# Kernel tuning notes

Hardware: AMD Instinct MI355X
Metric: run time of the kernel (lower is better)

The kernel has to match this reference:

```python
import jax, jax.numpy as jnp
import numpy as np
import math

B, T, D, H, V = 32, 512, 256, 4, 5000
NL = 6          # transformer layers
DUR_CAP = 8     # cap per-token duration so output length is static under jit
T_OUT = 2048    # fixed regulated length (avg duration ~1-2 with small init)


def _layernorm(x, g, b, eps=1e-5):
    m = jnp.mean(x, axis=-1, keepdims=True)
    v = jnp.var(x, axis=-1, keepdims=True)
    return (x - m) * jax.lax.rsqrt(v + eps) * g + b


def _conv1d(x, w, b):
    # x [B,C,T], w [O,I,K] -> [B,O,T], 'same' padding as in torch
    pad = (w.shape[-1] - 1) // 2
    y = jax.lax.conv_general_dilated(x, w, (1,), [(pad, pad)],
                                     dimension_numbers=('NCH', 'OIH', 'NCH'))
    return y + b[None, :, None]


def _pos_encoding(t, d):
    pos = jnp.arange(t, dtype=jnp.float32)[:, None]
    div = jnp.exp(jnp.arange(0, d, 2, dtype=jnp.float32) * (-math.log(10000.0) / d))
    ang = pos * div  # [t, d/2]
    return jnp.stack([jnp.sin(ang), jnp.cos(ang)], axis=-1).reshape(t, d)


def setup_inputs():
    key = jax.random.key(0)
    ks = iter(jax.random.split(key, 64))
    def nrm(shape, s=0.02):
        return jax.random.normal(next(ks), shape, dtype=jnp.float32) * s
    return {
        'text': jax.random.randint(next(ks), (B, T), 0, V, dtype=jnp.int32),
        'emotion': jax.random.normal(next(ks), (B, 1), dtype=jnp.float32),
        'emb': nrm((V, D), 1.0),
        'Wqkv': nrm((NL, D, 3 * D)), 'bqkv': jnp.zeros((NL, 3 * D)),
        'Wo': nrm((NL, D, D)), 'bo': jnp.zeros((NL, D)),
        'W1': nrm((NL, D, 4 * D)), 'b1': jnp.zeros((NL, 4 * D)),
        'W2': nrm((NL, 4 * D, D)), 'b2': jnp.zeros((NL, D)),
        'ln1g': jnp.ones((NL, D)), 'ln1b': jnp.zeros((NL, D)),
        'ln2g': jnp.ones((NL, D)), 'ln2b': jnp.zeros((NL, D)),
        'We1': nrm((1, 64), 0.1), 'be1': jnp.zeros((64,)),
        'We2': nrm((64, D), 0.1), 'be2': jnp.zeros((D,)),
        'dp_w1': nrm((D, D, 3)), 'dp_b1': jnp.zeros((D,)),
        'dp_g1': jnp.ones((D,)), 'dp_bt1': jnp.zeros((D,)),
        'dp_m1': jnp.zeros((D,)), 'dp_v1': jnp.ones((D,)),
        'dp_w2': nrm((D, D, 3)), 'dp_b2': jnp.zeros((D,)),
        'dp_g2': jnp.ones((D,)), 'dp_bt2': jnp.zeros((D,)),
        'dp_m2': jnp.zeros((D,)), 'dp_v2': jnp.ones((D,)),
        'dp_wo': nrm((1, D, 1)), 'dp_bo': jnp.zeros((1,)),
        'dec_w1': nrm((256, D, 5)), 'dec_b1': jnp.zeros((256,)),
        'dec_w2': nrm((128, 256, 5)), 'dec_b2': jnp.zeros((128,)),
        'dec_w3': nrm((1, 128, 5)), 'dec_b3': jnp.zeros((1,)),
    }


def reference(text, emotion, emb, Wqkv, bqkv, Wo, bo, W1, b1, W2, b2,
              ln1g, ln1b, ln2g, ln2b, We1, be1, We2, be2,
              dp_w1, dp_b1, dp_g1, dp_bt1, dp_m1, dp_v1,
              dp_w2, dp_b2, dp_g2, dp_bt2, dp_m2, dp_v2, dp_wo, dp_bo,
              dec_w1, dec_b1, dec_w2, dec_b2, dec_w3, dec_b3):
    dh = D // H
    scale = 1.0 / math.sqrt(dh)
    x = emb[text] + _pos_encoding(T, D)[None]  # [B,T,D]
    # post-norm TransformerEncoder (torch default), relu FFN, eval mode
    for i in range(NL):
        qkv = x @ Wqkv[i] + bqkv[i]
        q, k, v = jnp.split(qkv, 3, axis=-1)
        q = q.reshape(B, T, H, dh); k = k.reshape(B, T, H, dh); v = v.reshape(B, T, H, dh)
        att = jax.nn.softmax(jnp.einsum('bthd,bshd->bhts', q, k) * scale, axis=-1)
        o = jnp.einsum('bhts,bshd->bthd', att, v).reshape(B, T, D) @ Wo[i] + bo[i]
        x = _layernorm(x + o, ln1g[i], ln1b[i])
        ff = jax.nn.relu(x @ W1[i] + b1[i]) @ W2[i] + b2[i]
        x = _layernorm(x + ff, ln2g[i], ln2b[i])
    # EmotionFusion (assumed additive MLP projection, output_dim = 256)
    e = jax.nn.relu(emotion @ We1 + be1) @ We2 + be2  # [B,256]
    fused = x + e[:, None, :]                          # [B,T,D]
    # DurationPredictor (eval: BN with running stats, dropout off)
    def bn(y, g, bt, m, vv):
        return g[None, :, None] * (y - m[None, :, None]) * jax.lax.rsqrt(vv + 1e-5)[None, :, None] + bt[None, :, None]
    h = fused.transpose(0, 2, 1)  # [B,D,T]
    h = bn(jax.nn.relu(_conv1d(h, dp_w1, dp_b1)), dp_g1, dp_bt1, dp_m1, dp_v1)
    h = bn(jax.nn.relu(_conv1d(h, dp_w2, dp_b2)), dp_g2, dp_bt2, dp_m2, dp_v2)
    log_dur = _conv1d(h, dp_wo, dp_bo)[:, 0, :]  # [B,T]
    dur = jnp.clip(jnp.round(jnp.exp(log_dur)), 1, DUR_CAP).astype(jnp.int32)
    dur = jax.lax.stop_gradient(dur)
    # LengthRegulator: repeat token i dur[i] times, zero-pad to T_OUT
    def regulate(xb, db):
        total = jnp.sum(db)
        pad = jnp.maximum(T_OUT - total, 0)
        xe = jnp.concatenate([xb, jnp.zeros((1, D), xb.dtype)], axis=0)
        de = jnp.concatenate([db, pad[None]], axis=0)
        return jnp.repeat(xe, de, axis=0, total_repeat_length=T_OUT)
    reg = jax.vmap(regulate)(fused, dur)  # [B,T_OUT,D]
    # decoder conv stack
    y = reg.transpose(0, 2, 1)
    y = jax.nn.relu(_conv1d(y, dec_w1, dec_b1))
    y = jax.nn.relu(_conv1d(y, dec_w2, dec_b2))
    wav = _conv1d(y, dec_w3, dec_b3)[:, 0, :]  # [B,T_OUT]
    return wav
```

## Files before the change

kernel.cpp:

```cpp
#include <hip/hip_runtime.h>
#include <math.h>

#define NB 32
#define NT 512
#define ND 256
#define NH 4
#define NLAYER 6
#define TOUT 2048

typedef __attribute__((ext_vector_type(8))) short bf16x8;
typedef __attribute__((ext_vector_type(4))) float f32x4;
typedef __attribute__((ext_vector_type(16))) float f32x16;

static __device__ __forceinline__ unsigned short f2b(float f) {
    union { float f; unsigned int u; } x; x.f = f;
    unsigned int u = x.u;
    return (unsigned short)((u + 0x7FFFu + ((u >> 16) & 1u)) >> 16);
}
static __device__ __forceinline__ float b2f(unsigned short s) {
    union { unsigned int u; float f; } x; x.u = ((unsigned int)s) << 16;
    return x.f;
}

#define OFF_X    0ull
#define OFF_FFH  4194304ull
#define OFF_WBT  12582912ull
#define OFF_CWT  14942208ull
#define OFF_QKV  20971520ull
#define OFF_ATTN 33554432ull
#define OFF_PROJ 37748736ull
#define OFF_E    41943040ull
#define OFF_INT  41951232ull

__global__ __launch_bounds__(256) void embed_kernel(const int* __restrict__ text,
                                                    const float* __restrict__ emb,
                                                    float* __restrict__ x)
{
    const int row = blockIdx.x;
    const int d = threadIdx.x;
    const int t = row & (NT - 1);
    const int id = text[row];
    const int j2 = (d >> 1) * 2;
    const float c = -9.210340371976184f / 256.0f;
    float freq = expf((float)j2 * c);
    float ang = (float)t * freq;
    float pe = (d & 1) ? cosf(ang) : sinf(ang);
    x[(size_t)row * ND + d] = emb[(size_t)id * ND + d] + pe;
}

__global__ __launch_bounds__(256) void wq_kernel(const float* __restrict__ W,
                                                 unsigned short* __restrict__ out,
                                                 int K, int N, int inLS, int outLS)
{
    __shared__ float tile[32][33];
    const float* Wl = W + (size_t)blockIdx.z * inLS;
    unsigned short* ol = out + (size_t)blockIdx.z * outLS;
    const int n0 = blockIdx.x * 32, k0 = blockIdx.y * 32;
    const int tx = threadIdx.x & 31, ty = threadIdx.x >> 5;
#pragma unroll
    for (int j = 0; j < 4; ++j)
        tile[ty + j * 8][tx] = Wl[(size_t)(k0 + ty + j * 8) * N + n0 + tx];
    __syncthreads();
#pragma unroll
    for (int j = 0; j < 4; ++j)
        ol[(size_t)(n0 + ty + j * 8) * K + k0 + tx] = f2b(tile[tx][ty + j * 8]);
}

template<int NTILE, bool RELU, bool ABF16, bool CBF16>
__global__ __launch_bounds__(256) void gemmbf_kernel(const void* __restrict__ A_,
                                                     const unsigned short* __restrict__ Bt,
                                                     const float* __restrict__ bias,
                                                     void* __restrict__ C_,
                                                     int M, int N, int K)
{
    constexpr int MT = (NTILE == 128) ? 2 : 1;
    __shared__ __align__(16) unsigned short Asb[128 * 32];
    __shared__ __align__(16) unsigned short Bsb[NTILE * 32];
    const int tid = threadIdx.x;
    const int lane = tid & 63, wave = tid >> 6;
    const int ln = lane & 31, hi = lane >> 5;
    const int row0 = blockIdx.y * 128, col0 = blockIdx.x * NTILE;
    const int mOff = (NTILE == 128) ? (wave >> 1) * 64 : wave * 32;
    const int nOff = (NTILE == 128) ? (wave & 1) * 64 : 0;
    const float* Af = (const float*)A_;
    const unsigned short* Ab = (const unsigned short*)A_;
    float* Cf = (float*)C_;
    unsigned short* Cb = (unsigned short*)C_;
// ... 1 lines not shown

    for (int k0 = 0; k0 < K; k0 += 32) {
#pragma unroll
        for (int it = 0; it < 2; ++it) {
            int u = it * 256 + tid;
            int m = u >> 2, blk = u & 3;
            unsigned short s8[8];
            if (ABF16) {
                *(uint4*)s8 = *(const uint4*)&Ab[(size_t)(row0 + m) * K + k0 + blk * 8];
            } else {
                float4 v0 = *(const float4*)&Af[(size_t)(row0 + m) * K + k0 + blk * 8];
                float4 v1 = *(const float4*)&Af[(size_t)(row0 + m) * K + k0 + blk * 8 + 4];
                s8[0] = f2b(v0.x); s8[1] = f2b(v0.y); s8[2] = f2b(v0.z); s8[3] = f2b(v0.w);
                s8[4] = f2b(v1.x); s8[5] = f2b(v1.y); s8[6] = f2b(v1.z); s8[7] = f2b(v1.w);
            }
            *(uint4*)&Asb[m * 32 + ((blk ^ (m & 3)) << 3)] = *(uint4*)s8;
        }
#pragma unroll
        for (int it = 0; it < NTILE / 64; ++it) {
            int u = it * 256 + tid;
            int n = u >> 2, blk = u & 3;
            *(uint4*)&Bsb[n * 32 + ((blk ^ (n & 3)) << 3)] =
                *(const uint4*)&Bt[(size_t)(col0 + n) * K + k0 + blk * 8];
        }
        __syncthreads();
#pragma unroll
        for (int kh = 0; kh < 2; ++kh) {
            const int kb = kh * 2 + hi;
            bf16x8 af[MT], bfr[2];
#pragma unroll
            for (int mt = 0; mt < MT; ++mt) {
                int r = mOff + mt * 32 + ln;
                af[mt] = *(const bf16x8*)&Asb[r * 32 + ((kb ^ (r & 3)) << 3)];
            }
#pragma unroll
            for (int nt = 0; nt < 2; ++nt) {
                int r = nOff + nt * 32 + ln;
                bfr[nt] = *(const bf16x8*)&Bsb[r * 32 + ((kb ^ (r & 3)) << 3)];
            }
#pragma unroll
            for (int mt = 0; mt < MT; ++mt)
#pragma unroll
                for (int nt = 0; nt < 2; ++nt)
                    acc[mt][nt] = __builtin_amdgcn_mfma_f32_32x32x16_bf16(
                        af[mt], bfr[nt], acc[mt][nt], 0, 0, 0);
        }
        __syncthreads();
    }
#pragma unroll
    for (int mt = 0; mt < MT; ++mt)
#pragma unroll
        for (int nt = 0; nt < 2; ++nt) {
            int col = col0 + nOff + nt * 32 + ln;
            float bi = bias[col];
#pragma unroll
            for (int g = 0; g < 4; ++g)
#pragma unroll
                for (int r4 = 0; r4 < 4; ++r4) {
                    int row = row0 + mOff + mt * 32 + hi * 4 + g * 8 + r4;
                    float v = acc[mt][nt][g * 4 + r4] + bi;
                    if (RELU) v = fmaxf(v, 0.f);
                    if (CBF16) Cb[(size_t)row * N + col] = f2b(v);
                    else       Cf[(size_t)row * N + col] = v;
                }
        }
}

__global__ __launch_bounds__(256) void vtrans_kernel(const unsigned short* __restrict__ qkv,
                                                     unsigned short* __restrict__ vt)
{
    __shared__ unsigned short tile[64][65];
    const int t0 = blockIdx.x * 64, h = blockIdx.y, b = blockIdx.z;
    const int tid = threadIdx.x;
#pragma unroll
    for (int it = 0; it < 2; ++it) {
        int u = it * 256 + tid;
        int t = u >> 3, d8 = (u & 7) * 8;
        bf16x8 v = *(const bf16x8*)&qkv[((size_t)(b * NT) + t0 + t) * 768 + 512 + h * 64 + d8];
#pragma unroll
        for (int j = 0; j < 8; ++j) tile[t][d8 + j] = (unsigned short)v[j];
    }
    __syncthreads();
#pragma unroll
    for (int it = 0; it < 2; ++it) {
        int u = it * 256 + tid;
        int d = u >> 3, t8 = (u & 7) * 8;
        unsigned short s8[8];
#pragma unroll
        for (int j = 0; j < 8; ++j) s8[j] = tile[t8 + j][d];
        *(uint4*)&vt[((size_t)(b * NH + h) * 64 + d) * NT + t0 + t8] = *(uint4*)s8;
    }
}

__global__ __launch_bounds__(256, 2) void attn3_kernel(const unsigned short* __restrict__ qkv,
                                                       const unsigned short* __restrict__ vt,
                                                       unsigned short* __restrict__ out)
{
    __shared__ __align__(16) unsigned short sP[4][32 * 64];
    const int tid = threadIdx.x;
    const int lane = tid & 63, wave = tid >> 6;
    const int ln = lane & 31, hi = lane >> 5;
    const int h = blockIdx.y, b = blockIdx.z;
    const int q0 = blockIdx.x * 128 + wave * 32;
    const size_t base = (size_t)b * NT * 768;
    const int qoff = h * 64;
    const unsigned short* vbh = vt + (size_t)(b * NH + h) * 64 * NT;
// ... 100 lines not shown
#pragma unroll
    for (int o = 1; o < 64; o <<= 1) s += __shfl_xor(s, o);
    float m = s * (1.0f / 256.0f);
    float4 dv = make_float4(v.x - m, v.y - m, v.z - m, v.w - m);
    float s2 = dv.x * dv.x + dv.y * dv.y + dv.z * dv.z + dv.w * dv.w;
#pragma unroll
    for (int o = 1; o < 64; o <<= 1) s2 += __shfl_xor(s2, o);
    float r = 1.0f / sqrtf(s2 * (1.0f / 256.0f) + 1e-5f);
    float4 gv = *(const float4*)&g[c4];
    float4 bv = *(const float4*)&bta[c4];
    float4 o4 = make_float4(dv.x * r * gv.x + bv.x, dv.y * r * gv.y + bv.y,
                            dv.z * r * gv.z + bv.z, dv.w * r * gv.w + bv.w);
    *(float4*)&x[row * ND + c4] = o4;
}

__global__ __launch_bounds__(256) void emotion_kernel(const float* __restrict__ emo,
                                                      const float* __restrict__ We1,
                                                      const float* __restrict__ be1,
                                                      const float* __restrict__ We2,
                                                      const float* __restrict__ be2,
                                                      float* __restrict__ e)
{
    const int b = blockIdx.x, d = threadIdx.x;
    const float em = emo[b];
    float acc = be2[d];
    for (int j = 0; j < 64; ++j) {
        float h = fmaxf(em * We1[j] + be1[j], 0.0f);
        acc = fmaf(h, We2[j * ND + d], acc);
    }
    e[b * ND + d] = acc;
}

__global__ __launch_bounds__(256) void addfuse_kernel(float* __restrict__ x,
                                                      const float* __restrict__ e)
{
    const int row = blockIdx.x;
    const int d = threadIdx.x;
    x[(size_t)row * ND + d] += e[(row >> 9) * ND + d];
}

__global__ __launch_bounds__(256) void wtrans_kernel(const float* __restrict__ w,
                                                     float* __restrict__ wt,
                                                     int CIN, int COUT, int KS)
{
    int gid = blockIdx.x * 256 + threadIdx.x;
    int total = CIN * COUT * KS;
    if (gid >= total) return;
    int o = gid % COUT;
    int r = gid / COUT;
    int c = r % CIN;
    int k = r / CIN;
    wt[gid] = w[(o * CIN + c) * KS + k];
}

__global__ __launch_bounds__(256) void wtransb_kernel(const float* __restrict__ w,
                                                      unsigned short* __restrict__ wtb,
                                                      int CIN, int COUT, int KS)
{
    int gid = blockIdx.x * 256 + threadIdx.x;
    int total = CIN * COUT * KS;
    if (gid >= total) return;
    int c = gid % CIN;
    int r = gid / CIN;
    int o = r % COUT;
    int k = r / COUT;
    wtb[gid] = f2b(w[(o * CIN + c) * KS + k]);
}

template<int CIN, int KS, bool RELU, bool BN, bool GATHER>
__global__ __launch_bounds__(256, 4) void convg_kernel(const float* __restrict__ in,
                                                       const float* __restrict__ wt,
                                                       const float* __restrict__ bias,
                                                       const float* __restrict__ bng,
                                                       const float* __restrict__ bnb,
                                                       const float* __restrict__ bnm,
                                                       const float* __restrict__ bnv,
                                                       const int* __restrict__ tok,
                                                       float* __restrict__ out,
                                                       int T, int in_T, int COUT)
{
    constexpr int TM = 128;
    constexpr int PAD = (KS - 1) / 2;
    constexpr int TEXT = TM + KS - 1;
    constexpr int PITCH = (TEXT + 3) & ~3;
    __shared__ __align__(16) float As[16 * PITCH];
    __shared__ __align__(16) float Bs[16 * KS * 68];
    const int tid = threadIdx.x;
    const int lane = tid & 63, wave = tid >> 6;
    const int b = blockIdx.z;
    const int t0 = blockIdx.x * TM;
    const int o0 = blockIdx.y * 64;
    const int wt0 = wave * 32;
    const int r0 = (lane >> 3) << 2;
    const int c0 = (lane & 7) << 2;
    float acc[4][8] = {};

    for (int cc = 0; cc < CIN; cc += 16) {
        for (int i = tid; i < TEXT * 4; i += 256) {
            int t = i >> 2, q = i & 3;
            int tg = t0 - PAD + t;
            float4 v = make_float4(0.f, 0.f, 0.f, 0.f);
            if (tg >= 0 && tg < T) {
                long row;
                if (GATHER) {
                    int tk = tok[b * T + tg];
                    row = (tk >= 0) ? ((long)b * in_T + tk) : -1;
                } else {
                    row = (long)b * T + tg;
                }
                if (row >= 0) v = *(const float4*)&in[row * CIN + cc + (q << 2)];
            }
            As[((q << 2) + 0) * PITCH + t] = v.x;
            As[((q << 2) + 1) * PITCH + t] = v.y;
            As[((q << 2) + 2) * PITCH + t] = v.z;
            As[((q << 2) + 3) * PITCH + t] = v.w;
        }
        for (int i = tid; i < KS * 256; i += 256) {
            int row = i >> 4, o4 = (i & 15) << 2;
            int k = row >> 4, ci = row & 15;
            *(float4*)&Bs[row * 68 + o4] =
                *(const float4*)&wt[(size_t)(k * CIN + cc + ci) * COUT + o0 + o4];
        }
        __syncthreads();
#pragma unroll 2
        for (int ci = 0; ci < 16; ++ci) {
            float a[8];
            float4 A0 = *(const float4*)&As[ci * PITCH + wt0 + r0];
            float4 A1 = *(const float4*)&As[ci * PITCH + wt0 + r0 + 4];
            a[0] = A0.x; a[1] = A0.y; a[2] = A0.z; a[3] = A0.w;
            a[4] = A1.x; a[5] = A1.y; a[6] = A1.z; a[7] = A1.w;
#pragma unroll
            for (int k = 0; k < KS; ++k) {
                float4 b0 = *(const float4*)&Bs[(k * 16 + ci) * 68 + c0];
                float4 b1 = *(const float4*)&Bs[(k * 16 + ci) * 68 + 32 + c0];
                float bb[8] = {b0.x, b0.y, b0.z, b0.w, b1.x, b1.y, b1.z, b1.w};
#pragma unroll
                for (int i = 0; i < 4; ++i)
#pragma unroll
                    for (int j = 0; j < 8; ++j)
                        acc[i][j] = fmaf(a[i + k], bb[j], acc[i][j]);
            }
        }
        __syncthreads();
    }

    float4 bi0 = *(const float4*)(bias + o0 + c0);
    float4 bi1 = *(const float4*)(bias + o0 + 32 + c0);
    float bb[8] = {bi0.x, bi0.y, bi0.z, bi0.w, bi1.x, bi1.y, bi1.z, bi1.w};
    float sc[8], sh[8];
    if (BN) {
        float4 g0 = *(const float4*)(bng + o0 + c0);
        float4 g1 = *(const float4*)(bng + o0 + 32 + c0);
        float4 t0v = *(const float4*)(bnb + o0 + c0);
        float4 t1v = *(const float4*)(bnb + o0 + 32 + c0);
        float4 m0 = *(const float4*)(bnm + o0 + c0);
        float4 m1 = *(const float4*)(bnm + o0 + 32 + c0);
        float4 v0 = *(const float4*)(bnv + o0 + c0);
        float4 v1 = *(const float4*)(bnv + o0 + 32 + c0);
        float gg[8] = {g0.x, g0.y, g0.z, g0.w, g1.x, g1.y, g1.z, g1.w};
        float tb[8] = {t0v.x, t0v.y, t0v.z, t0v.w, t1v.x, t1v.y, t1v.z, t1v.w};
        float mm[8] = {m0.x, m0.y, m0.z, m0.w, m1.x, m1.y, m1.z, m1.w};
        float vv[8] = {v0.x, v0.y, v0.z, v0.w, v1.x, v1.y, v1.z, v1.w};
#pragma unroll
        for (int j = 0; j < 8; ++j) {
            sc[j] = gg[j] / sqrtf(vv[j] + 1e-5f);
            sh[j] = tb[j] - mm[j] * sc[j];
        }
    }
#pragma unroll
    for (int i = 0; i < 4; ++i) {
        int r = t0 + wt0 + r0 + i;
#pragma unroll
        for (int jh = 0; jh < 2; ++jh) {
            float o4[4];
#pragma unroll
            for (int j = 0; j < 4; ++j) {
                float yv = acc[i][jh * 4 + j] + bb[jh * 4 + j];
                if (RELU) yv = fmaxf(yv, 0.0f);
                if (BN) yv = yv * sc[jh * 4 + j] + sh[jh * 4 + j];
                o4[j] = yv;
            }
            *(float4*)&out[((size_t)b * T + r) * COUT + o0 + jh * 32 + c0] =
                make_float4(o4[0], o4[1], o4[2], o4[3]);
        }
    }
}

__global__ __launch_bounds__(256) void reg_kernel(const float* __restrict__ x,
                                                  const int* __restrict__ tok,
                                                  unsigned short* __restrict__ reg)
{
    const int wave = threadIdx.x >> 6, lane = threadIdx.x & 63;
    const int row = blockIdx.x * 4 + wave;
    const int tk = tok[row];
    const int b = row >> 11;
    const int c4 = lane * 4;
    unsigned short s4[4] = {0, 0, 0, 0};
    if (tk >= 0) {
        float4 v = *(const float4*)&x[((size_t)(b * NT) + tk) * ND + c4];
        s4[0] = f2b(v.x); s4[1] = f2b(v.y); s4[2] = f2b(v.z); s4[3] = f2b(v.w);
    }
    *(uint2*)&reg[(size_t)row * ND + c4] = *(uint2*)s4;
}

template<int CIN, int KS, bool RELU>
__global__ __launch_bounds__(256) void convmf2_kernel(const unsigned short* __restrict__ in,
                                                      const unsigned short* __restrict__ wtb,
                                                      const float* __restrict__ bias,
                                                      unsigned short* __restrict__ out,
                                                      int T, int COUT)
{
    constexpr int PAD = (KS - 1) / 2;
    constexpr int TEXT = 128 + KS - 1;
    __shared__ __align__(16) unsigned short Asb[TEXT * 32];
    __shared__ __align__(16) unsigned short Bsb[KS * 64 * 32];
    const int tid = threadIdx.x;
    const int lane = tid & 63, wave = tid >> 6;
    const int ln = lane & 31, hi = lane >> 5;
    const int b = blockIdx.z;
    const int t0 = blockIdx.x * 128;
    const int o0 = blockIdx.y * 64;
    const int mOff = wave * 32;
    f32x16 acc[2] = {};

    for (int cc = 0; cc < CIN; cc += 32) {
        for (int u = tid; u < TEXT * 4; u += 256) {
            int t = u >> 2, blk = u & 3;
            int tg = t0 - PAD + t;
            uint4 v = make_uint4(0, 0, 0, 0);
            if (tg >= 0 && tg < T)
                v = *(const uint4*)&in[((size_t)(b * T) + tg) * CIN + cc + blk * 8];
            *(uint4*)&Asb[t * 32 + ((blk ^ (t & 3)) << 3)] = v;
        }
        for (int u = tid; u < KS * 256; u += 256) {
            int row = u >> 2, blk = u & 3;
            int k = row >> 6, o = row & 63;
            *(uint4*)&Bsb[row * 32 + ((blk ^ (row & 3)) << 3)] =
                *(const uint4*)&wtb[((size_t)k * COUT + o0 + o) * CIN + cc + blk * 8];
        }
        __syncthreads();
#pragma unroll
        for (int kh = 0; kh < 2; ++kh) {
            const int kb = kh * 2 + hi;
            bf16x8 af[KS];
#pragma unroll
            for (int tap = 0; tap < KS; ++tap) {
                int r = mOff + ln + tap;
                af[tap] = *(const bf16x8*)&Asb[r * 32 + ((kb ^ (r & 3)) << 3)];
            }
#pragma unroll
            for (int nt = 0; nt < 2; ++nt) {
                int rb = nt * 32 + ln;
#pragma unroll
                for (int tap = 0; tap < KS; ++tap) {
                    bf16x8 bfr = *(const bf16x8*)&Bsb[(tap * 64 + rb) * 32 + ((kb ^ (rb & 3)) << 3)];
                    acc[nt] = __builtin_amdgcn_mfma_f32_32x32x16_bf16(af[tap], bfr, acc[nt], 0, 0, 0);
                }
            }
        }
        __syncthreads();
    }
#pragma unroll
    for (int nt = 0; nt < 2; ++nt) {
        int col = o0 + nt * 32 + ln;
        float bi = bias[col];
#pragma unroll
        for (int g = 0; g < 4; ++g)
#pragma unroll
            for (int r4 = 0; r4 < 4; ++r4) {
                int row = t0 + mOff + hi * 4 + g * 8 + r4;
                float v = acc[nt][g * 4 + r4] + bi;
                if (RELU) v = fmaxf(v, 0.f);
                out[((size_t)(b * T) + row) * COUT + col] = f2b(v);
            }
    }
}

__global__ __launch_bounds__(256) void dur_kernel(const float* __restrict__ h2,
                                                  const float* __restrict__ wo,
                                                  const float* __restrict__ bo,
                                                  int* __restrict__ dur)
{
    const int wave = threadIdx.x >> 6, lane = threadIdx.x & 63;
    const int row = blockIdx.x * 4 + wave;
    const int c4 = lane * 4;
    float4 h = *(const float4*)&h2[(size_t)row * ND + c4];
    float4 w4 = *(const float4*)&wo[c4];
    float s = h.x * w4.x + h.y * w4.y + h.z * w4.z + h.w * w4.w;
#pragma unroll
    for (int o = 1; o < 64; o <<= 1) s += __shfl_xor(s, o);
    if (lane == 0) {
        float d = rintf(expf(s + bo[0]));
        d = fminf(fmaxf(d, 1.0f), 8.0f);
        dur[row] = (int)d;
    }
}

__global__ __launch_bounds__(64) void scan_kernel(const int* __restrict__ dur,
                                                  int* __restrict__ starts,
                                                  int* __restrict__ totals)
{
    const int b = threadIdx.x;
    if (b >= NB) return;
    int acc = 0;
    for (int t = 0; t < NT; ++t) {
        starts[b * NT + t] = acc;
        acc += dur[b * NT + t];
    }
    totals[b] = acc;
}

__global__ __launch_bounds__(256) void tok_kernel(const int* __restrict__ starts,
                                                  const int* __restrict__ totals,
                                                  int* __restrict__ tok)
{
    const int gid = blockIdx.x * 256 + threadIdx.x;
    const int b = gid >> 11, p = gid & (TOUT - 1);
    const int total = totals[b];
    int res = -1;
    if (p < total) {
        const int* st = starts + b * NT;
        int lo = 0, hi = NT - 1;
        while (lo < hi) {
            int mid = (lo + hi + 1) >> 1;
            if (st[mid] <= p) lo = mid; else hi = mid - 1;
        }
        res = lo;
    }
    tok[gid] = res;
}

__global__ __launch_bounds__(256) void conv3_kernel(const unsigned short* __restrict__ in,
                                                    const float* __restrict__ w,
                                                    const float* __restrict__ bias,
                                                    float* __restrict__ out)
{
    const int wave = threadIdx.x >> 6, lane = threadIdx.x & 63;
    const int gid = blockIdx.x * 4 + wave;
    const int b = gid >> 11, t = gid & (TOUT - 1);
    const int c = lane * 2;
    float w0[5], w1[5];
#pragma unroll
    for (int k = 0; k < 5; ++k) { w0[k] = w[c * 5 + k]; w1[k] = w[(c + 1) * 5 + k]; }
    float acc = 0.f;
// ... 35 lines not shown
    const float* be2     = (const float*)d_in[18];
    const float* dp_w1   = (const float*)d_in[19];
    const float* dp_b1   = (const float*)d_in[20];
    const float* dp_g1   = (const float*)d_in[21];
    const float* dp_bt1  = (const float*)d_in[22];
    const float* dp_m1   = (const float*)d_in[23];
    const float* dp_v1   = (const float*)d_in[24];
    const float* dp_w2   = (const float*)d_in[25];
    const float* dp_b2   = (const float*)d_in[26];
    const float* dp_g2   = (const float*)d_in[27];
    const float* dp_bt2  = (const float*)d_in[28];
    const float* dp_m2   = (const float*)d_in[29];
    const float* dp_v2   = (const float*)d_in[30];
    const float* dp_wo   = (const float*)d_in[31];
    const float* dp_bo   = (const float*)d_in[32];
    const float* dec_w1  = (const float*)d_in[33];
    const float* dec_b1  = (const float*)d_in[34];
    const float* dec_w2  = (const float*)d_in[35];
    const float* dec_b2  = (const float*)d_in[36];
    const float* dec_w3  = (const float*)d_in[37];
    const float* dec_b3  = (const float*)d_in[38];

    float* ws   = (float*)d_ws;
    float* x    = ws + OFF_X;
    unsigned short* ffhB = (unsigned short*)(ws + OFF_FFH);
    unsigned short* Wbt  = (unsigned short*)(ws + OFF_WBT);
    float* wtdp1 = ws + OFF_CWT;
    float* wtdp2 = wtdp1 + 196608;
    unsigned short* wtb1 = (unsigned short*)(wtdp2 + 196608);
    unsigned short* wtb2 = wtb1 + 327680;
    unsigned short* qkvB = (unsigned short*)(ws + OFF_QKV);
    unsigned short* vtb  = qkvB + 12582912;
    unsigned short* regB = qkvB;
    float* attb = ws + OFF_ATTN;
    float* prjb = ws + OFF_PROJ;
    float* ebuf = ws + OFF_E;
    unsigned short* attbB = (unsigned short*)attb;
    unsigned short* d1b  = ffhB;
    unsigned short* d2b  = (unsigned short*)attb;
    int*   ip     = (int*)(ws + OFF_INT);
    int*   durb   = ip;
    int*   startb = ip + 16384;
    int*   totb   = ip + 32768;
    int*   tokb   = ip + 32832;

    const int M = NB * NT;

    embed_kernel<<<M, 256, 0, stream>>>(text, emb, x);

    wq_kernel<<<dim3(24, 8, 6), 256, 0, stream>>>(Wqkv, Wbt + 0,      256, 768,  196608, 786432);
    wq_kernel<<<dim3(8,  8, 6), 256, 0, stream>>>(Wo,   Wbt + 196608, 256, 256,  65536,  786432);
    wq_kernel<<<dim3(32, 8, 6), 256, 0, stream>>>(W1,   Wbt + 262144, 256, 1024, 262144, 786432);
    wq_kernel<<<dim3(8, 32, 6), 256, 0, stream>>>(W2,   Wbt + 524288, 1024, 256, 262144, 786432);

    for (int l = 0; l < NLAYER; ++l) {
        const unsigned short* WQ  = Wbt + (size_t)l * 786432;
        const unsigned short* WO  = WQ + 196608;
        const unsigned short* WF1 = WQ + 262144;
        const unsigned short* WF2 = WQ + 524288;
        gemmbf_kernel<128, false, false, true><<<dim3(6, 128), 256, 0, stream>>>(
            x, WQ, bqkv + l * 768, qkvB, M, 768, 256);
        vtrans_kernel<<<dim3(NT / 64, NH, NB), 256, 0, stream>>>(qkvB, vtb);
        attn3_kernel<<<dim3(NT / 128, NH, NB), 256, 0, stream>>>(qkvB, vtb, attbB);
        gemmbf_kernel<64, false, true, false><<<dim3(4, 128), 256, 0, stream>>>(
            attbB, WO, bo + l * 256, prjb, M, 256, 256);
        add_ln_kernel<<<M / 4, 256, 0, stream>>>(x, prjb, ln1g + l * ND, ln1b + l * ND);
        gemmbf_kernel<128, true, false, true><<<dim3(8, 128), 256, 0, stream>>>(
            x, WF1, b1 + l * 1024, ffhB, M, 1024, 256);
        gemmbf_kernel<64, false, true, false><<<dim3(4, 128), 256, 0, stream>>>(
            ffhB, WF2, b2 + l * 256, prjb, M, 256, 1024);
        add_ln_kernel<<<M / 4, 256, 0, stream>>>(x, prjb, ln2g + l * ND, ln2b + l * ND);
    }

    emotion_kernel<<<NB, 256, 0, stream>>>(emotion, We1, be1, We2, be2, ebuf);
    addfuse_kernel<<<M, 256, 0, stream>>>(x, ebuf);

    wtrans_kernel<<<(256 * 256 * 3 + 255) / 256, 256, 0, stream>>>(dp_w1, wtdp1, 256, 256, 3);
    wtrans_kernel<<<(256 * 256 * 3 + 255) / 256, 256, 0, stream>>>(dp_w2, wtdp2, 256, 256, 3);
    wtransb_kernel<<<(256 * 256 * 5 + 255) / 256, 256, 0, stream>>>(dec_w1, wtb1, 256, 256, 5);
    wtransb_kernel<<<(128 * 256 * 5 + 255) / 256, 256, 0, stream>>>(dec_w2, wtb2, 256, 128, 5);

    convg_kernel<256, 3, true, true, false><<<dim3(NT / 128, 4, NB), 256, 0, stream>>>(
        x, wtdp1, dp_b1, dp_g1, dp_bt1, dp_m1, dp_v1, nullptr, attb, NT, NT, 256);
    convg_kernel<256, 3, true, true, false><<<dim3(NT / 128, 4, NB), 256, 0, stream>>>(
        attb, wtdp2, dp_b2, dp_g2, dp_bt2, dp_m2, dp_v2, nullptr, prjb, NT, NT, 256);
    dur_kernel<<<M / 4, 256, 0, stream>>>(prjb, dp_wo, dp_bo, durb);
    scan_kernel<<<1, 64, 0, stream>>>(durb, startb, totb);
    tok_kernel<<<NB * TOUT / 256, 256, 0, stream>>>(startb, totb, tokb);

    reg_kernel<<<NB * TOUT / 4, 256, 0, stream>>>(x, tokb, regB);
    convmf2_kernel<256, 5, true><<<dim3(TOUT / 128, 4, NB), 256, 0, stream>>>(
        regB, wtb1, dec_b1, d1b, TOUT, 256);
    convmf2_kernel<256, 5, true><<<dim3(TOUT / 128, 2, NB), 256, 0, stream>>>(
        d1b, wtb2, dec_b2, d2b, TOUT, 128);
    conv3_kernel<<<NB * TOUT / 4, 256, 0, stream>>>(d2b, dec_w3, dec_b3, (float*)d_out);
}
```

Measured before the change: 1.619 ms.

## Fuse V transpose into QKV GEMM, move duration convs to MFMA, merge prep kernels

The QKV GEMM epilogue now writes V directly in transposed layout, which removes the separate vtrans kernel. The fp32 duration-predictor convolutions are replaced by a unified bf16 MFMA conv kernel that is also used for the decoder convs. Weight-prep launches are merged into single kernels, emotion is fused into the add, and scan plus token lookup become one per-batch kernel. The LDS swizzle in the GEMM also changes. Together these cut launch count and memory traffic, at the cost of bf16 precision in the duration path, which could flip rounded durations.

```diff
diff --git a/kernel.cpp b/kernel.cpp
--- a/kernel.cpp
+++ b/kernel.cpp
@@ -21,6 +21,8 @@
     union { unsigned int u; float f; } x; x.u = ((unsigned int)s) << 16;
     return x.f;
 }
+
+#define SW(r) (((r) >> 1) & 3)
 
 #define OFF_X    0ull
 #define OFF_FFH  4194304ull
@@ -29,7 +31,6 @@
 #define OFF_QKV  20971520ull
 #define OFF_ATTN 33554432ull
 #define OFF_PROJ 37748736ull
-#define OFF_E    41943040ull
 #define OFF_INT  41951232ull
 
 __global__ __launch_bounds__(256) void embed_kernel(const int* __restrict__ text,
@@ -48,14 +49,21 @@
     x[(size_t)row * ND + d] = emb[(size_t)id * ND + d] + pe;
 }
 
-__global__ __launch_bounds__(256) void wq_kernel(const float* __restrict__ W,
-                                                 unsigned short* __restrict__ out,
-                                                 int K, int N, int inLS, int outLS)
+__global__ __launch_bounds__(256) void wqall_kernel(const float* __restrict__ Wqkv,
+                                                    const float* __restrict__ Wo,
+                                                    const float* __restrict__ W1,
+                                                    const float* __restrict__ W2,
+                                                    unsigned short* __restrict__ Wbt)
 {
     __shared__ float tile[32][33];
-    const float* Wl = W + (size_t)blockIdx.z * inLS;
-    unsigned short* ol = out + (size_t)blockIdx.z * outLS;
-    const int n0 = blockIdx.x * 32, k0 = blockIdx.y * 32;
+    const int tt = blockIdx.x, layer = blockIdx.y;
+    const float* src; int K, N, n0, k0, inLS; size_t outSeg;
+    if (tt < 192)      { src = Wqkv; K = 256;  N = 768;  n0 = (tt % 24) * 32; k0 = (tt / 24) * 32; inLS = 196608; outSeg = 0; }
+    else if (tt < 256) { int t2 = tt - 192; src = Wo; K = 256; N = 256;  n0 = (t2 & 7) * 32;  k0 = (t2 >> 3) * 32; inLS = 65536;  outSeg = 196608; }
+    else if (tt < 512) { int t3 = tt - 256; src = W1; K = 256; N = 1024; n0 = (t3 & 31) * 32; k0 = (t3 >> 5) * 32; inLS = 262144; outSeg = 262144; }
+    else               { int t4 = tt - 512; src = W2; K = 1024; N = 256; n0 = (t4 & 7) * 32;  k0 = (t4 >> 3) * 32; inLS = 262144; outSeg = 524288; }
+    const float* Wl = src + (size_t)layer * inLS;
+    unsigned short* ol = Wbt + (size_t)layer * 786432 + outSeg;
     const int tx = threadIdx.x & 31, ty = threadIdx.x >> 5;
 #pragma unroll
     for (int j = 0; j < 4; ++j)
@@ -66,11 +74,32 @@
         ol[(size_t)(n0 + ty + j * 8) * K + k0 + tx] = f2b(tile[tx][ty + j * 8]);
 }
 
-template<int NTILE, bool RELU, bool ABF16, bool CBF16>
+__global__ __launch_bounds__(256) void wtransball_kernel(const float* __restrict__ dp_w1,
+                                                         const float* __restrict__ dp_w2,
+                                                         const float* __restrict__ dec_w1,
+                                                         const float* __restrict__ dec_w2,
+                                                         unsigned short* __restrict__ cw)
+{
+    int gid = blockIdx.x * 256 + threadIdx.x;
+    if (gid >= 884736) return;
+    const float* src; int CIN = 256, COUT, KS, idx;
+    if (gid < 196608)      { src = dp_w1;  COUT = 256; KS = 3; idx = gid; }
+    else if (gid < 393216) { src = dp_w2;  COUT = 256; KS = 3; idx = gid - 196608; }
+    else if (gid < 720896) { src = dec_w1; COUT = 256; KS = 5; idx = gid - 393216; }
+    else                   { src = dec_w2; COUT = 128; KS = 5; idx = gid - 720896; }
+    int c = idx % CIN;
+    int r = idx / CIN;
+    int o = r % COUT;
+    int k = r / COUT;
+    cw[gid] = f2b(src[(o * CIN + c) * KS + k]);
+}
+
+template<int NTILE, bool RELU, bool ABF16, bool CBF16, bool VOUT>
 __global__ __launch_bounds__(256) void gemmbf_kernel(const void* __restrict__ A_,
                                                      const unsigned short* __restrict__ Bt,
                                                      const float* __restrict__ bias,
                                                      void* __restrict__ C_,
+                                                     unsigned short* __restrict__ vt,
                                                      int M, int N, int K)
 {
     constexpr int MT = (NTILE == 128) ? 2 : 1;
@@ -102,13 +131,13 @@
                 s8[0] = f2b(v0.x); s8[1] = f2b(v0.y); s8[2] = f2b(v0.z); s8[3] = f2b(v0.w);
                 s8[4] = f2b(v1.x); s8[5] = f2b(v1.y); s8[6] = f2b(v1.z); s8[7] = f2b(v1.w);
             }
-            *(uint4*)&Asb[m * 32 + ((blk ^ (m & 3)) << 3)] = *(uint4*)s8;
+            *(uint4*)&Asb[m * 32 + ((blk ^ SW(m)) << 3)] = *(uint4*)s8;
         }
 #pragma unroll
         for (int it = 0; it < NTILE / 64; ++it) {
             int u = it * 256 + tid;
             int n = u >> 2, blk = u & 3;
-            *(uint4*)&Bsb[n * 32 + ((blk ^ (n & 3)) << 3)] =
+            *(uint4*)&Bsb[n * 32 + ((blk ^ SW(n)) << 3)] =
                 *(const uint4*)&Bt[(size_t)(col0 + n) * K + k0 + blk * 8];
         }
         __syncthreads();
@@ -119,12 +148,12 @@
 #pragma unroll
             for (int mt = 0; mt < MT; ++mt) {
                 int r = mOff + mt * 32 + ln;
-                af[mt] = *(const bf16x8*)&Asb[r * 32 + ((kb ^ (r & 3)) << 3)];
+                af[mt] = *(const bf16x8*)&Asb[r * 32 + ((kb ^ SW(r)) << 3)];
             }
 #pragma unroll
             for (int nt = 0; nt < 2; ++nt) {
                 int r = nOff + nt * 32 + ln;
-                bfr[nt] = *(const bf16x8*)&Bsb[r * 32 + ((kb ^ (r & 3)) << 3)];
+                bfr[nt] = *(const bf16x8*)&Bsb[r * 32 + ((kb ^ SW(r)) << 3)];
             }
 #pragma unroll
             for (int mt = 0; mt < MT; ++mt)
@@ -142,42 +171,24 @@
             int col = col0 + nOff + nt * 32 + ln;
             float bi = bias[col];
 #pragma unroll
-            for (int g = 0; g < 4; ++g)
+            for (int g = 0; g < 4; ++g) {
+                unsigned short s4[4];
 #pragma unroll
                 for (int r4 = 0; r4 < 4; ++r4) {
                     int row = row0 + mOff + mt * 32 + hi * 4 + g * 8 + r4;
                     float v = acc[mt][nt][g * 4 + r4] + bi;
                     if (RELU) v = fmaxf(v, 0.f);
-                    if (CBF16) Cb[(size_t)row * N + col] = f2b(v);
+                    if (CBF16) { s4[r4] = f2b(v); Cb[(size_t)row * N + col] = s4[r4]; }
                     else       Cf[(size_t)row * N + col] = v;
                 }
-        }
-}
-
-__global__ __launch_bounds__(256) void vtrans_kernel(const unsigned short* __restrict__ qkv,
-                                                     unsigned short* __restrict__ vt)
-{
-    __shared__ unsigned short tile[64][65];
-    const int t0 = blockIdx.x * 64, h = blockIdx.y, b = blockIdx.z;
-    const int tid = threadIdx.x;
-#pragma unroll
-    for (int it = 0; it < 2; ++it) {
-        int u = it * 256 + tid;
-        int t = u >> 3, d8 = (u & 7) * 8;
-        bf16x8 v = *(const bf16x8*)&qkv[((size_t)(b * NT) + t0 + t) * 768 + 512 + h * 64 + d8];
-#pragma unroll
-        for (int j = 0; j < 8; ++j) tile[t][d8 + j] = (unsigned short)v[j];
-    }
-    __syncthreads();
-#pragma unroll
-    for (int it = 0; it < 2; ++it) {
-        int u = it * 256 + tid;
-        int d = u >> 3, t8 = (u & 7) * 8;
-        unsigned short s8[8];
-#pragma unroll
-        for (int j = 0; j < 8; ++j) s8[j] = tile[t8 + j][d];
-        *(uint4*)&vt[((size_t)(b * NH + h) * 64 + d) * NT + t0 + t8] = *(uint4*)s8;
-    }
+                if (VOUT && col >= 512) {
+                    int rowg = row0 + mOff + mt * 32 + hi * 4 + g * 8;
+                    int b = rowg >> 9, t = rowg & (NT - 1);
+                    int hh = (col - 512) >> 6, dd = (col - 512) & 63;
+                    *(uint2*)&vt[((size_t)(b * NH + hh) * 64 + dd) * NT + t] = *(uint2*)s4;
+                }
+            }
+        }
 }
 
 __global__ __launch_bounds__(256, 2) void attn3_kernel(const unsigned short* __restrict__ qkv,
@@ -308,201 +319,34 @@
     *(float4*)&x[row * ND + c4] = o4;
 }
 
-__global__ __launch_bounds__(256) void emotion_kernel(const float* __restrict__ emo,
-                                                      const float* __restrict__ We1,
-                                                      const float* __restrict__ be1,
-                                                      const float* __restrict__ We2,
-                                                      const float* __restrict__ be2,
-                                                      float* __restrict__ e)
-{
-    const int b = blockIdx.x, d = threadIdx.x;
-    const float em = emo[b];
+__global__ __launch_bounds__(256) void fuse_kernel(const float* __restrict__ emo,
+                                                   const float* __restrict__ We1,
+                                                   const float* __restrict__ be1,
+                                                   const float* __restrict__ We2,
+                                                   const float* __restrict__ be2,
+                                                   float* __restrict__ x)
+{
+    const int row = blockIdx.x;
+    const int d = threadIdx.x;
+    const float em = emo[row >> 9];
     float acc = be2[d];
     for (int j = 0; j < 64; ++j) {
         float h = fmaxf(em * We1[j] + be1[j], 0.0f);
         acc = fmaf(h, We2[j * ND + d], acc);
     }
-    e[b * ND + d] = acc;
-}
-
-__global__ __launch_bounds__(256) void addfuse_kernel(float* __restrict__ x,
-                                                      const float* __restrict__ e)
-{
-    const int row = blockIdx.x;
-    const int d = threadIdx.x;
-    x[(size_t)row * ND + d] += e[(row >> 9) * ND + d];
-}
-
-__global__ __launch_bounds__(256) void wtrans_kernel(const float* __restrict__ w,
-                                                     float* __restrict__ wt,
-                                                     int CIN, int COUT, int KS)
-{
-    int gid = blockIdx.x * 256 + threadIdx.x;
-    int total = CIN * COUT * KS;
-    if (gid >= total) return;
-    int o = gid % COUT;
-    int r = gid / COUT;
-    int c = r % CIN;
-    int k = r / CIN;
-    wt[gid] = w[(o * CIN + c) * KS + k];
-}
-
-__global__ __launch_bounds__(256) void wtransb_kernel(const float* __restrict__ w,
-                                                      unsigned short* __restrict__ wtb,
-                                                      int CIN, int COUT, int KS)
-{
-    int gid = blockIdx.x * 256 + threadIdx.x;
-    int total = CIN * COUT * KS;
-    if (gid >= total) return;
-    int c = gid % CIN;
-    int r = gid / CIN;
-    int o = r % COUT;
-    int k = r / COUT;
-    wtb[gid] = f2b(w[(o * CIN + c) * KS + k]);
-}
-
-template<int CIN, int KS, bool RELU, bool BN, bool GATHER>
-__global__ __launch_bounds__(256, 4) void convg_kernel(const float* __restrict__ in,
-                                                       const float* __restrict__ wt,
-                                                       const float* __restrict__ bias,
-                                                       const float* __restrict__ bng,
-                                                       const float* __restrict__ bnb,
-                                                       const float* __restrict__ bnm,
-                                                       const float* __restrict__ bnv,
-                                                       const int* __restrict__ tok,
-                                                       float* __restrict__ out,
-                                                       int T, int in_T, int COUT)
-{
-    constexpr int TM = 128;
-    constexpr int PAD = (KS - 1) / 2;
-    constexpr int TEXT = TM + KS - 1;
-    constexpr int PITCH = (TEXT + 3) & ~3;
-    __shared__ __align__(16) float As[16 * PITCH];
-    __shared__ __align__(16) float Bs[16 * KS * 68];
-    const int tid = threadIdx.x;
-    const int lane = tid & 63, wave = tid >> 6;
-    const int b = blockIdx.z;
-    const int t0 = blockIdx.x * TM;
-    const int o0 = blockIdx.y * 64;
-    const int wt0 = wave * 32;
-    const int r0 = (lane >> 3) << 2;
-    const int c0 = (lane & 7) << 2;
-    float acc[4][8] = {};
-
-    for (int cc = 0; cc < CIN; cc += 16) {
-        for (int i = tid; i < TEXT * 4; i += 256) {
-            int t = i >> 2, q = i & 3;
-            int tg = t0 - PAD + t;
-            float4 v = make_float4(0.f, 0.f, 0.f, 0.f);
-            if (tg >= 0 && tg < T) {
-                long row;
-                if (GATHER) {
-                    int tk = tok[b * T + tg];
-                    row = (tk >= 0) ? ((long)b * in_T + tk) : -1;
-                } else {
-                    row = (long)b * T + tg;
-                }
-                if (row >= 0) v = *(const float4*)&in[row * CIN + cc + (q << 2)];
-            }
-            As[((q << 2) + 0) * PITCH + t] = v.x;
-            As[((q << 2) + 1) * PITCH + t] = v.y;
-            As[((q << 2) + 2) * PITCH + t] = v.z;
-            As[((q << 2) + 3) * PITCH + t] = v.w;
-        }
-        for (int i = tid; i < KS * 256; i += 256) {
-            int row = i >> 4, o4 = (i & 15) << 2;
-            int k = row >> 4, ci = row & 15;
-            *(float4*)&Bs[row * 68 + o4] =
-                *(const float4*)&wt[(size_t)(k * CIN + cc + ci) * COUT + o0 + o4];
-        }
-        __syncthreads();
-#pragma unroll 2
-        for (int ci = 0; ci < 16; ++ci) {
-            float a[8];
-            float4 A0 = *(const float4*)&As[ci * PITCH + wt0 + r0];
-            float4 A1 = *(const float4*)&As[ci * PITCH + wt0 + r0 + 4];
-            a[0] = A0.x; a[1] = A0.y; a[2] = A0.z; a[3] = A0.w;
-            a[4] = A1.x; a[5] = A1.y; a[6] = A1.z; a[7] = A1.w;
-#pragma unroll
-            for (int k = 0; k < KS; ++k) {
-                float4 b0 = *(const float4*)&Bs[(k * 16 + ci) * 68 + c0];
-                float4 b1 = *(const float4*)&Bs[(k * 16 + ci) * 68 + 32 + c0];
-                float bb[8] = {b0.x, b0.y, b0.z, b0.w, b1.x, b1.y, b1.z, b1.w};
-#pragma unroll
-                for (int i = 0; i < 4; ++i)
-#pragma unroll
-                    for (int j = 0; j < 8; ++j)
-                        acc[i][j] = fmaf(a[i + k], bb[j], acc[i][j]);
-            }
-        }
-        __syncthreads();
-    }
-
-    float4 bi0 = *(const float4*)(bias + o0 + c0);
-    float4 bi1 = *(const float4*)(bias + o0 + 32 + c0);
-    float bb[8] = {bi0.x, bi0.y, bi0.z, bi0.w, bi1.x, bi1.y, bi1.z, bi1.w};
-    float sc[8], sh[8];
-    if (BN) {
-        float4 g0 = *(const float4*)(bng + o0 + c0);
-        float4 g1 = *(const float4*)(bng + o0 + 32 + c0);
-        float4 t0v = *(const float4*)(bnb + o0 + c0);
-        float4 t1v = *(const float4*)(bnb + o0 + 32 + c0);
-        float4 m0 = *(const float4*)(bnm + o0 + c0);
-        float4 m1 = *(const float4*)(bnm + o0 + 32 + c0);
-        float4 v0 = *(const float4*)(bnv + o0 + c0);
-        float4 v1 = *(const float4*)(bnv + o0 + 32 + c0);
-        float gg[8] = {g0.x, g0.y, g0.z, g0.w, g1.x, g1.y, g1.z, g1.w};
-        float tb[8] = {t0v.x, t0v.y, t0v.z, t0v.w, t1v.x, t1v.y, t1v.z, t1v.w};
-        float mm[8] = {m0.x, m0.y, m0.z, m0.w, m1.x, m1.y, m1.z, m1.w};
-        float vv[8] = {v0.x, v0.y, v0.z, v0.w, v1.x, v1.y, v1.z, v1.w};
-#pragma unroll
-        for (int j = 0; j < 8; ++j) {
-            sc[j] = gg[j] / sqrtf(vv[j] + 1e-5f);
-            sh[j] = tb[j] - mm[j] * sc[j];
-        }
-    }
-#pragma unroll
-    for (int i = 0; i < 4; ++i) {
-        int r = t0 + wt0 + r0 + i;
-#pragma unroll
-        for (int jh = 0; jh < 2; ++jh) {
-            float o4[4];
-#pragma unroll
-            for (int j = 0; j < 4; ++j) {
-                float yv = acc[i][jh * 4 + j] + bb[jh * 4 + j];
-                if (RELU) yv = fmaxf(yv, 0.0f);
-                if (BN) yv = yv * sc[jh * 4 + j] + sh[jh * 4 + j];
-                o4[j] = yv;
-            }
-            *(float4*)&out[((size_t)b * T + r) * COUT + o0 + jh * 32 + c0] =
-                make_float4(o4[0], o4[1], o4[2], o4[3]);
-        }
-    }
-}
-
-__global__ __launch_bounds__(256) void reg_kernel(const float* __restrict__ x,
-                                                  const int* __restrict__ tok,
-                                                  unsigned short* __restrict__ reg)
-{
-    const int wave = threadIdx.x >> 6, lane = threadIdx.x & 63;
-    const int row = blockIdx.x * 4 + wave;
-    const int tk = tok[row];
-    const int b = row >> 11;
-    const int c4 = lane * 4;
-    unsigned short s4[4] = {0, 0, 0, 0};
-    if (tk >= 0) {
-        float4 v = *(const float4*)&x[((size_t)(b * NT) + tk) * ND + c4];
-        s4[0] = f2b(v.x); s4[1] = f2b(v.y); s4[2] = f2b(v.z); s4[3] = f2b(v.w);
-    }
-    *(uint2*)&reg[(size_t)row * ND + c4] = *(uint2*)s4;
-}
-
-template<int CIN, int KS, bool RELU>
-__global__ __launch_bounds__(256) void convmf2_kernel(const unsigned short* __restrict__ in,
-                                                      const unsigned short* __restrict__ wtb,
-                                                      const float* __restrict__ bias,
-                                                      unsigned short* __restrict__ out,
-                                                      int T, int COUT)
+    x[(size_t)row * ND + d] += acc;
+}
+
+template<int CIN, int KS, bool IN_BF16, bool OUT_BF16, bool BN>
+__global__ __launch_bounds__(256) void convk_kernel(const void* __restrict__ in_,
+                                                    const unsigned short* __restrict__ wtb,
+                                                    const float* __restrict__ bias,
+                                                    const float* __restrict__ bng,
+                                                    const float* __restrict__ bnb,
+                                                    const float* __restrict__ bnm,
+                                                    const float* __restrict__ bnv,
+                                                    void* __restrict__ out_,
+                                                    int T, int COUT)
 {
     constexpr int PAD = (KS - 1) / 2;
     constexpr int TEXT = 128 + KS - 1;
@@ -515,21 +359,33 @@
     const int t0 = blockIdx.x * 128;
     const int o0 = blockIdx.y * 64;
     const int mOff = wave * 32;
+    const float* inf = (const float*)in_;
+    const unsigned short* inb = (const unsigned short*)in_;
+    float* outf = (float*)out_;
+    unsigned short* outb = (unsigned short*)out_;
     f32x16 acc[2] = {};
 
     for (int cc = 0; cc < CIN; cc += 32) {
         for (int u = tid; u < TEXT * 4; u += 256) {
             int t = u >> 2, blk = u & 3;
             int tg = t0 - PAD + t;
-            uint4 v = make_uint4(0, 0, 0, 0);
-            if (tg >= 0 && tg < T)
-                v = *(const uint4*)&in[((size_t)(b * T) + tg) * CIN + cc + blk * 8];
-            *(uint4*)&Asb[t * 32 + ((blk ^ (t & 3)) << 3)] = v;
+            unsigned short s8[8] = {0, 0, 0, 0, 0, 0, 0, 0};
+            if (tg >= 0 && tg < T) {
+                if (IN_BF16) {
+                    *(uint4*)s8 = *(const uint4*)&inb[((size_t)(b * T) + tg) * CIN + cc + blk * 8];
+                } else {
+                    float4 v0 = *(const float4*)&inf[((size_t)(b * T) + tg) * CIN + cc + blk * 8];
+                    float4 v1 = *(const float4*)&inf[((size_t)(b * T) + tg) * CIN + cc + blk * 8 + 4];
+                    s8[0] = f2b(v0.x); s8[1] = f2b(v0.y); s8[2] = f2b(v0.z); s8[3] = f2b(v0.w);
+                    s8[4] = f2b(v1.x); s8[5] = f2b(v1.y); s8[6] = f2b(v1.z); s8[7] = f2b(v1.w);
+                }
+            }
+            *(uint4*)&Asb[t * 32 + ((blk ^ SW(t)) << 3)] = *(uint4*)s8;
         }
         for (int u = tid; u < KS * 256; u += 256) {
             int row = u >> 2, blk = u & 3;
             int k = row >> 6, o = row & 63;
-            *(uint4*)&Bsb[row * 32 + ((blk ^ (row & 3)) << 3)] =
+            *(uint4*)&Bsb[row * 32 + ((blk ^ SW(row)) << 3)] =
                 *(const uint4*)&wtb[((size_t)k * COUT + o0 + o) * CIN + cc + blk * 8];
         }
         __syncthreads();
@@ -540,14 +396,14 @@
 #pragma unroll
             for (int tap = 0; tap < KS; ++tap) {
                 int r = mOff + ln + tap;
-                af[tap] = *(const bf16x8*)&Asb[r * 32 + ((kb ^ (r & 3)) << 3)];
+                af[tap] = *(const bf16x8*)&Asb[r * 32 + ((kb ^ SW(r)) << 3)];
             }
 #pragma unroll
             for (int nt = 0; nt < 2; ++nt) {
-                int rb = nt * 32 + ln;
 #pragma unroll
                 for (int tap = 0; tap < KS; ++tap) {
-                    bf16x8 bfr = *(const bf16x8*)&Bsb[(tap * 64 + rb) * 32 + ((kb ^ (rb & 3)) << 3)];
+                    int rb = tap * 64 + nt * 32 + ln;
+                    bf16x8 bfr = *(const bf16x8*)&Bsb[rb * 32 + ((kb ^ SW(rb)) << 3)];
                     acc[nt] = __builtin_amdgcn_mfma_f32_32x32x16_bf16(af[tap], bfr, acc[nt], 0, 0, 0);
                 }
             }
@@ -558,16 +414,39 @@
     for (int nt = 0; nt < 2; ++nt) {
         int col = o0 + nt * 32 + ln;
         float bi = bias[col];
+        float scv = 1.f, shv = 0.f;
+        if (BN) {
+            scv = bng[col] / sqrtf(bnv[col] + 1e-5f);
+            shv = bnb[col] - bnm[col] * scv;
+        }
 #pragma unroll
         for (int g = 0; g < 4; ++g)
 #pragma unroll
             for (int r4 = 0; r4 < 4; ++r4) {
                 int row = t0 + mOff + hi * 4 + g * 8 + r4;
-                float v = acc[nt][g * 4 + r4] + bi;
-                if (RELU) v = fmaxf(v, 0.f);
-                out[((size_t)(b * T) + row) * COUT + col] = f2b(v);
-            }
-    }
+                float v = fmaxf(acc[nt][g * 4 + r4] + bi, 0.f);
+                if (BN) v = v * scv + shv;
+                if (OUT_BF16) outb[((size_t)(b * T) + row) * COUT + col] = f2b(v);
+                else          outf[((size_t)(b * T) + row) * COUT + col] = v;
+            }
+    }
+}
+
+__global__ __launch_bounds__(256) void reg_kernel(const float* __restrict__ x,
+                                                  const int* __restrict__ tok,
+                                                  unsigned short* __restrict__ reg)
+{
+    const int wave = threadIdx.x >> 6, lane = threadIdx.x & 63;
+    const int row = blockIdx.x * 4 + wave;
+    const int tk = tok[row];
+    const int b = row >> 11;
+    const int c4 = lane * 4;
+    unsigned short s4[4] = {0, 0, 0, 0};
+    if (tk >= 0) {
+        float4 v = *(const float4*)&x[((size_t)(b * NT) + tk) * ND + c4];
+        s4[0] = f2b(v.x); s4[1] = f2b(v.y); s4[2] = f2b(v.z); s4[3] = f2b(v.w);
+    }
+    *(uint2*)&reg[(size_t)row * ND + c4] = *(uint2*)s4;
 }
 
 __global__ __launch_bounds__(256) void dur_kernel(const float* __restrict__ h2,
@@ -590,38 +469,30 @@
     }
 }
 
-__global__ __launch_bounds__(64) void scan_kernel(const int* __restrict__ dur,
-                                                  int* __restrict__ starts,
-                                                  int* __restrict__ totals)
-{
-    const int b = threadIdx.x;
-    if (b >= NB) return;
-    int acc = 0;
-    for (int t = 0; t < NT; ++t) {
-        starts[b * NT + t] = acc;
-        acc += dur[b * NT + t];
-    }
-    totals[b] = acc;
-}
-
-__global__ __launch_bounds__(256) void tok_kernel(const int* __restrict__ starts,
-                                                  const int* __restrict__ totals,
-                                                  int* __restrict__ tok)
-{
-    const int gid = blockIdx.x * 256 + threadIdx.x;
-    const int b = gid >> 11, p = gid & (TOUT - 1);
-    const int total = totals[b];
-    int res = -1;
-    if (p < total) {
-        const int* st = starts + b * NT;
-        int lo = 0, hi = NT - 1;
-        while (lo < hi) {
-            int mid = (lo + hi + 1) >> 1;
-            if (st[mid] <= p) lo = mid; else hi = mid - 1;
-        }
-        res = lo;
-    }
-    tok[gid] = res;
+__global__ __launch_bounds__(256) void scantok_kernel(const int* __restrict__ dur,
+                                                      int* __restrict__ tok)
+{
+    __shared__ int st[NT];
+    __shared__ int tot;
+    const int b = blockIdx.x, tid = threadIdx.x;
+    if (tid == 0) {
+        int a = 0;
+        for (int t = 0; t < NT; ++t) { st[t] = a; a += dur[b * NT + t]; }
+        tot = a;
+    }
+    __syncthreads();
+    for (int p = tid; p < TOUT; p += 256) {
+        int res = -1;
+        if (p < tot) {
+            int lo = 0, hi = NT - 1;
+            while (lo < hi) {
+                int mid = (lo + hi + 1) >> 1;
+                if (st[mid] <= p) lo = mid; else hi = mid - 1;
+            }
+            res = lo;
+        }
+        tok[b * TOUT + p] = res;
+    }
 }
 
 __global__ __launch_bounds__(256) void conv3_kernel(const unsigned short* __restrict__ in,
@@ -687,84 +558,71 @@
     const float* dp_v2   = (const float*)d_in[30];
     const float* dp_wo   = (const float*)d_in[31];
     const float* dp_bo   = (const float*)d_in[32];
-    const float* dec_w1  = (const float*)d_in[33];
+    const float* dec_w3  = (const float*)d_in[37];
     const float* dec_b1  = (const float*)d_in[34];
-    const float* dec_w2  = (const float*)d_in[35];
     const float* dec_b2  = (const float*)d_in[36];
-    const float* dec_w3  = (const float*)d_in[37];
     const float* dec_b3  = (const float*)d_in[38];
 
     float* ws   = (float*)d_ws;
     float* x    = ws + OFF_X;
     unsigned short* ffhB = (unsigned short*)(ws + OFF_FFH);
     unsigned short* Wbt  = (unsigned short*)(ws + OFF_WBT);
-    float* wtdp1 = ws + OFF_CWT;
-    float* wtdp2 = wtdp1 + 196608;
-    unsigned short* wtb1 = (unsigned short*)(wtdp2 + 196608);
-    unsigned short* wtb2 = wtb1 + 327680;
+    unsigned short* cw   = (unsigned short*)(ws + OFF_CWT);
+    unsigned short* wtbdp1 = cw;
+    unsigned short* wtbdp2 = cw + 196608;
+    unsigned short* wtb1   = cw + 393216;
+    unsigned short* wtb2   = cw + 720896;
     unsigned short* qkvB = (unsigned short*)(ws + OFF_QKV);
     unsigned short* vtb  = qkvB + 12582912;
     unsigned short* regB = qkvB;
     float* attb = ws + OFF_ATTN;
     float* prjb = ws + OFF_PROJ;
-    float* ebuf = ws + OFF_E;
     unsigned short* attbB = (unsigned short*)attb;
+    unsigned short* h1b  = (unsigned short*)attb;
     unsigned short* d1b  = ffhB;
     unsigned short* d2b  = (unsigned short*)attb;
     int*   ip     = (int*)(ws + OFF_INT);
     int*   durb   = ip;
-    int*   startb = ip + 16384;
-    int*   totb   = ip + 32768;
-    int*   tokb   = ip + 32832;
+    int*   tokb   = ip + 16384;
 
     const int M = NB * NT;
 
     embed_kernel<<<M, 256, 0, stream>>>(text, emb, x);
-
-    wq_kernel<<<dim3(24, 8, 6), 256, 0, stream>>>(Wqkv, Wbt + 0,      256, 768,  196608, 786432);
-    wq_kernel<<<dim3(8,  8, 6), 256, 0, stream>>>(Wo,   Wbt + 196608, 256, 256,  65536,  786432);
-    wq_kernel<<<dim3(32, 8, 6), 256, 0, stream>>>(W1,   Wbt + 262144, 256, 1024, 262144, 786432);
-    wq_kernel<<<dim3(8, 32, 6), 256, 0, stream>>>(W2,   Wbt + 524288, 1024, 256, 262144, 786432);
+    wqall_kernel<<<dim3(768, 6), 256, 0, stream>>>(Wqkv, Wo, W1, W2, Wbt);
+    wtransball_kernel<<<3456, 256, 0, stream>>>(dp_w1, dp_w2,
+                                                (const float*)d_in[33], (const float*)d_in[35], cw);
 
     for (int l = 0; l < NLAYER; ++l) {
         const unsigned short* WQ  = Wbt + (size_t)l * 786432;
         const unsigned short* WO  = WQ + 196608;
         const unsigned short* WF1 = WQ + 262144;
         const unsigned short* WF2 = WQ + 524288;
-        gemmbf_kernel<128, false, false, true><<<dim3(6, 128), 256, 0, stream>>>(
-            x, WQ, bqkv + l * 768, qkvB, M, 768, 256);
-        vtrans_kernel<<<dim3(NT / 64, NH, NB), 256, 0, stream>>>(qkvB, vtb);
+        gemmbf_kernel<128, false, false, true, true><<<dim3(6, 128), 256, 0, stream>>>(
+            x, WQ, bqkv + l * 768, qkvB, vtb, M, 768, 256);
         attn3_kernel<<<dim3(NT / 128, NH, NB), 256, 0, stream>>>(qkvB, vtb, attbB);
-        gemmbf_kernel<64, false, true, false><<<dim3(4, 128), 256, 0, stream>>>(
-            attbB, WO, bo + l * 256, prjb, M, 256, 256);
+        gemmbf_kernel<64, false, true, false, false><<<dim3(4, 128), 256, 0, stream>>>(
+            attbB, WO, bo + l * 256, prjb, nullptr, M, 256, 256);
         add_ln_kernel<<<M / 4, 256, 0, stream>>>(x, prjb, ln1g + l * ND, ln1b + l * ND);
-        gemmbf_kernel<128, true, false, true><<<dim3(8, 128), 256, 0, stream>>>(
-            x, WF1, b1 + l * 1024, ffhB, M, 1024, 256);
-        gemmbf_kernel<64, false, true, false><<<dim3(4, 128), 256, 0, stream>>>(
-            ffhB, WF2, b2 + l * 256, prjb, M, 256, 1024);
+        gemmbf_kernel<128, true, false, true, false><<<dim3(8, 128), 256, 0, stream>>>(
+            x, WF1, b1 + l * 1024, ffhB, nullptr, M, 1024, 256);
+        gemmbf_kernel<64, false, true, false, false><<<dim3(4, 128), 256, 0, stream>>>(
+            ffhB, WF2, b2 + l * 256, prjb, nullptr, M, 256, 1024);
         add_ln_kernel<<<M / 4, 256, 0, stream>>>(x, prjb, ln2g + l * ND, ln2b + l * ND);
     }
 
-    emotion_kernel<<<NB, 256, 0, stream>>>(emotion, We1, be1, We2, be2, ebuf);
-    addfuse_kernel<<<M, 256, 0, stream>>>(x, ebuf);
-
-    wtrans_kernel<<<(256 * 256 * 3 + 255) / 256, 256, 0, stream>>>(dp_w1, wtdp1, 256, 256, 3);
-    wtrans_kernel<<<(256 * 256 * 3 + 255) / 256, 256, 0, stream>>>(dp_w2, wtdp2, 256, 256, 3);
-    wtransb_kernel<<<(256 * 256 * 5 + 255) / 256, 256, 0, stream>>>(dec_w1, wtb1, 256, 256, 5);
-    wtransb_kernel<<<(128 * 256 * 5 + 255) / 256, 256, 0, stream>>>(dec_w2, wtb2, 256, 128, 5);
-
-    convg_kernel<256, 3, true, true, false><<<dim3(NT / 128, 4, NB), 256, 0, stream>>>(
-        x, wtdp1, dp_b1, dp_g1, dp_bt1, dp_m1, dp_v1, nullptr, attb, NT, NT, 256);
-    convg_kernel<256, 3, true, true, false><<<dim3(NT / 128, 4, NB), 256, 0, stream>>>(
-        attb, wtdp2, dp_b2, dp_g2, dp_bt2, dp_m2, dp_v2, nullptr, prjb, NT, NT, 256);
+    fuse_kernel<<<M, 256, 0, stream>>>(emotion, We1, be1, We2, be2, x);
+
+    convk_kernel<256, 3, false, true, true><<<dim3(4, 4, NB), 256, 0, stream>>>(
+        x, wtbdp1, dp_b1, dp_g1, dp_bt1, dp_m1, dp_v1, h1b, NT, 256);
+    convk_kernel<256, 3, true, false, true><<<dim3(4, 4, NB), 256, 0, stream>>>(
+        h1b, wtbdp2, dp_b2, dp_g2, dp_bt2, dp_m2, dp_v2, prjb, NT, 256);
     dur_kernel<<<M / 4, 256, 0, stream>>>(prjb, dp_wo, dp_bo, durb);
-    scan_kernel<<<1, 64, 0, stream>>>(durb, startb, totb);
-    tok_kernel<<<NB * TOUT / 256, 256, 0, stream>>>(startb, totb, tokb);
+    scantok_kernel<<<NB, 256, 0, stream>>>(durb, tokb);
 
     reg_kernel<<<NB * TOUT / 4, 256, 0, stream>>>(x, tokb, regB);
-    convmf2_kernel<256, 5, true><<<dim3(TOUT / 128, 4, NB), 256, 0, stream>>>(
-        regB, wtb1, dec_b1, d1b, TOUT, 256);
-    convmf2_kernel<256, 5, true><<<dim3(TOUT / 128, 2, NB), 256, 0, stream>>>(
-        d1b, wtb2, dec_b2, d2b, TOUT, 128);
+    convk_kernel<256, 5, true, true, false><<<dim3(TOUT / 128, 4, NB), 256, 0, stream>>>(
+        regB, wtb1, dec_b1, nullptr, nullptr, nullptr, nullptr, d1b, TOUT, 256);
+    convk_kernel<256, 5, true, true, false><<<dim3(TOUT / 128, 2, NB), 256, 0, stream>>>(
+        d1b, wtb2, dec_b2, nullptr, nullptr, nullptr, nullptr, d2b, TOUT, 128);
     conv3_kernel<<<NB * TOUT / 4, 256, 0, stream>>>(d2b, dec_w3, dec_b3, (float*)d_out);
 }
```

New measurement: 1.498 ms. 7.5% less time.
